# Optimization experiments

Hardware: AMD Instinct MI355X
Metric: run time of the kernel (lower is better)

## Reference

```python
import jax, jax.numpy as jnp
import numpy as np

N_NODES = 100000
N_EDGES = 1600000
EMD_DIM = 64
EPS = 1e-12  # F.normalize eps


def setup_inputs() -> dict:
    key = jax.random.key(0)
    ks = jax.random.split(key, 7)
    x = jax.random.normal(ks[0], (N_NODES, EMD_DIM), dtype=jnp.float32)
    W = jax.random.normal(ks[1], (EMD_DIM, EMD_DIM), dtype=jnp.float32) * (1.0 / np.sqrt(EMD_DIM))
    b = jax.random.normal(ks[2], (EMD_DIM,), dtype=jnp.float32) * 0.02
    wc = jax.random.normal(ks[3], (EMD_DIM,), dtype=jnp.float32) * (1.0 / np.sqrt(EMD_DIM))
    bc = jax.random.normal(ks[4], (1,), dtype=jnp.float32) * 0.02
    src = jax.random.randint(ks[5], (N_EDGES,), 0, N_NODES, dtype=jnp.int32)
    dst = jax.random.randint(ks[6], (N_EDGES,), 0, N_NODES, dtype=jnp.int32)
    return {"x": x, "W": W, "b": b, "wc": wc, "bc": bc, "src": src, "dst": dst}


def reference(x, W, b, wc, bc, src, dst):
    # gnn2: DGL GraphConv(norm='none', activation=None):
    #   y = sum_{(u->v) in E} (x @ W)[u]  scattered into v, plus bias.
    y = x @ W                                   # [N, D] dense transform first (D small)
    msg = y[src]                                # [E, D] gather
    agg = jax.ops.segment_sum(msg, dst, num_segments=x.shape[0])  # [N, D] scatter-add
    h = agg + b
    # F.normalize(h, p=2, dim=1)
    norm = jnp.linalg.norm(h, axis=1, keepdims=True)
    h = h / jnp.maximum(norm, EPS)
    # dgl.mean_nodes -> mean over all nodes; classifier Linear(D, 1).squeeze(-1)
    graph_repr = jnp.mean(h, axis=0)            # [D]
    logits = graph_repr @ wc + bc[0]            # scalar
    # emb dict is just contiguous slices of h (h2dict); h carries all embeddings.
    return logits, h
```

## Files before the change

kernel.cpp:

```cpp
#include <hip/hip_runtime.h>

#define NN 100000
#define NE 1600000
#define D 64
#define NB ((NN + 255) / 256)
#define SCAN2_T 512

__global__ __launch_bounds__(256) void degree_hist(const int* __restrict__ dst,
                                                   int* __restrict__ deg) {
    const int n4 = NE / 4;
    for (int i = blockIdx.x * blockDim.x + threadIdx.x; i < n4;
         i += gridDim.x * blockDim.x) {
        const int4 d = reinterpret_cast<const int4*>(dst)[i];
        atomicAdd(&deg[d.x], 1);
        atomicAdd(&deg[d.y], 1);
        atomicAdd(&deg[d.z], 1);
        atomicAdd(&deg[d.w], 1);
    }
}

__global__ __launch_bounds__(256) void scan1(const int* __restrict__ deg,
                                             int* __restrict__ partial,
                                             int* __restrict__ blockSums) {
    const int t = threadIdx.x;
    const int i = blockIdx.x * 256 + t;
    const int lane = t & 63, wid = t >> 6;
    const int orig = (i < NN) ? deg[i] : 0;
    int v = orig;
#pragma unroll
    for (int off = 1; off < 64; off <<= 1) {
        int n = __shfl_up(v, off, 64);
        if (lane >= off) v += n;
    }
    __shared__ int wsum[4];
    if (lane == 63) wsum[wid] = v;
    __syncthreads();
    if (t == 0) {
        int s = 0;
#pragma unroll
        for (int w = 0; w < 4; ++w) { int tmp = wsum[w]; wsum[w] = s; s += tmp; }
    }
    __syncthreads();
    const int incl = v + wsum[wid];
    if (i < NN) partial[i] = incl - orig;
    if (t == 255) blockSums[blockIdx.x] = incl;
}

__global__ __launch_bounds__(SCAN2_T) void scan2(int* __restrict__ blockSums) {
    __shared__ int sm[SCAN2_T];
    const int t = threadIdx.x;
    const int orig = (t < NB) ? blockSums[t] : 0;
    sm[t] = orig;
    __syncthreads();
    for (int off = 1; off < SCAN2_T; off <<= 1) {
        int v = (t >= off) ? sm[t - off] : 0;
        __syncthreads();
        sm[t] += v;
        __syncthreads();
    }
    if (t < NB) blockSums[t] = sm[t] - orig;
}

__global__ __launch_bounds__(256) void scan3(const int* __restrict__ partial,
                                             const int* __restrict__ blockSums,
                                             int* __restrict__ offs,
                                             int* __restrict__ cursor) {
    const int i = blockIdx.x * 256 + threadIdx.x;
    if (i < NN) {
        const int o = partial[i] + blockSums[blockIdx.x];
        offs[i] = o;
        cursor[i] = o;
    }
}

__global__ __launch_bounds__(256) void bucket_fill(const int* __restrict__ src,
                                                   const int* __restrict__ dst,
                                                   int* __restrict__ cursor,
                                                   int* __restrict__ csr) {
    const int n4 = NE / 4;
    for (int i = blockIdx.x * blockDim.x + threadIdx.x; i < n4;
         i += gridDim.x * blockDim.x) {
        const int4 d = reinterpret_cast<const int4*>(dst)[i];
        const int4 s = reinterpret_cast<const int4*>(src)[i];
        __builtin_nontemporal_store(s.x, &csr[atomicAdd(&cursor[d.x], 1)]);
        __builtin_nontemporal_store(s.y, &csr[atomicAdd(&cursor[d.y], 1)]);
        __builtin_nontemporal_store(s.z, &csr[atomicAdd(&cursor[d.z], 1)]);
        __builtin_nontemporal_store(s.w, &csr[atomicAdd(&cursor[d.w], 1)]);
    }
}

__global__ __launch_bounds__(256) void gather_transform_norm(
        const float* __restrict__ x, const int* __restrict__ csr,
        const int* __restrict__ offs, const int* __restrict__ deg,
        const float* __restrict__ W, const float* __restrict__ b,
        float* __restrict__ h, float* __restrict__ colsum) {
    const int lane = threadIdx.x & 63;
    const int wid  = threadIdx.x >> 6;
    const int grp  = lane >> 4;
    const int sub  = lane & 15;

    __shared__ float Wt[64 * 65];
    __shared__ float smem[4][64];
    for (int idx = threadIdx.x; idx < 64 * 64; idx += 256) {
        const int k = idx >> 6, l = idx & 63;
        Wt[l * 65 + k] = W[idx];
    }
    __syncthreads();
    const float bj = b[lane];
    const float* wrow = &Wt[lane * 65];

    const int waveId = (blockIdx.x * blockDim.x + threadIdx.x) >> 6;
    const int nWaves = (gridDim.x * blockDim.x) >> 6;
    float csum = 0.f;
    for (int node = waveId; node < NN; node += nWaves) {
        const int start = offs[node];
        const int cnt   = deg[node];
        float ax = 0.f, ay = 0.f, az = 0.f, aw = 0.f;
        for (int c0 = 0; c0 < cnt; c0 += 64) {
            const int pos  = start + c0 + lane;
            const int idxv = (pos < NE) ? csr[pos] : 0;
            const int m = (cnt - c0 < 64) ? (cnt - c0) : 64;
#pragma unroll 4
            for (int j = 0; j < m; j += 4) {
                const int e = j + grp;
                const int s = __shfl(idxv, e, 64);
                if (e < m) {
                    const float4 v = *reinterpret_cast<const float4*>(
                        x + (size_t)s * D + 4 * sub);
                    ax += v.x; ay += v.y; az += v.z; aw += v.w;
                }
            }
        }
#pragma unroll
        for (int off = 16; off <= 32; off <<= 1) {
            ax += __shfl_xor(ax, off, 64);
            ay += __shfl_xor(ay, off, 64);
            az += __shfl_xor(az, off, 64);
            aw += __shfl_xor(aw, off, 64);
        }
        float v = bj;
#pragma unroll
        for (int k0 = 0; k0 < 16; ++k0) {
            const float a0 = __shfl(ax, k0, 64);
            const float a1 = __shfl(ay, k0, 64);
            const float a2 = __shfl(az, k0, 64);
            const float a3 = __shfl(aw, k0, 64);
            v = fmaf(a0, wrow[4 * k0 + 0], v);
            v = fmaf(a1, wrow[4 * k0 + 1], v);
            v = fmaf(a2, wrow[4 * k0 + 2], v);
            v = fmaf(a3, wrow[4 * k0 + 3], v);
        }
        float ss = v * v;
#pragma unroll
        for (int off = 32; off > 0; off >>= 1) ss += __shfl_xor(ss, off, 64);
        v = v / fmaxf(sqrtf(ss), 1e-12f);
        __builtin_nontemporal_store(v, &h[(size_t)node * D + lane]);
        csum += v;
    }
    smem[wid][lane] = csum;
    __syncthreads();
    if (wid == 0) {
        const float t = smem[0][lane] + smem[1][lane] + smem[2][lane] + smem[3][lane];
        atomicAdd(&colsum[lane], t);
    }
}

__global__ void finalize(const float* __restrict__ colsum,
                         const float* __restrict__ wc,
                         const float* __restrict__ bc,
                         float* __restrict__ out0) {
    const int lane = threadIdx.x;
    float v = colsum[lane] * (1.0f / (float)NN) * wc[lane];
#pragma unroll
    for (int off = 32; off > 0; off >>= 1) v += __shfl_xor(v, off, 64);
    if (lane == 0) out0[0] = v + bc[0];
}

extern "C" void kernel_launch(void* const* d_in, const int* in_sizes, int n_in,
                              void* d_out, int out_size, void* d_ws, size_t ws_size,
                              hipStream_t stream) {
    const float* x   = (const float*)d_in[0];
    const float* W   = (const float*)d_in[1];
    const float* b   = (const float*)d_in[2];
    const float* wc  = (const float*)d_in[3];
    const float* bc  = (const float*)d_in[4];
    const int*   src = (const int*)d_in[5];
    const int*   dst = (const int*)d_in[6];

    float* out = (float*)d_out;
    float* h   = out + 1;

    int*   deg       = (int*)d_ws;
    int*   partial   = deg + NN;
    int*   offs      = partial + NN;
    int*   cursor    = offs + NN;
    int*   blockSums = cursor + NN;
    float* colsum    = (float*)(blockSums + SCAN2_T);
    int*   csr       = (int*)(colsum + 64);

    hipMemsetAsync(deg, 0, NN * sizeof(int), stream);
    hipMemsetAsync(colsum, 0, 64 * sizeof(float), stream);

    degree_hist<<<2048, 256, 0, stream>>>(dst, deg);
    scan1<<<NB, 256, 0, stream>>>(deg, partial, blockSums);
    scan2<<<1, SCAN2_T, 0, stream>>>(blockSums);
    scan3<<<NB, 256, 0, stream>>>(partial, blockSums, offs, cursor);
    bucket_fill<<<2048, 256, 0, stream>>>(src, dst, cursor, csr);
    gather_transform_norm<<<4096, 256, 0, stream>>>(x, csr, offs, deg, W, b, h, colsum);
    finalize<<<1, 64, 0, stream>>>(colsum, wc, bc, out);
}
```

Baseline: 438.3 us.

## Fuse CSR build phases into one cooperative kernel with grid syncs

Replaces the two memsets and five separate kernels (degree histogram, three-stage scan, bucket fill) with a single cooperative kernel of 512 blocks of 512 threads that separates the phases with grid.sync(). The aim is to remove per-launch overhead and inter-kernel gaps across the small phases. It also switches the nontemporal stores for csr and h to ordinary stores. In exchange, grid-wide barriers cost time, and the fixed grid gives less parallelism to the atomic-heavy phases than the earlier 2048-block launches.

```diff
diff --git a/kernel.cpp b/kernel.cpp
--- a/kernel.cpp
+++ b/kernel.cpp
@@ -1,91 +1,102 @@
 #include <hip/hip_runtime.h>
+#include <hip/hip_cooperative_groups.h>
+
+namespace cg = cooperative_groups;
 
 #define NN 100000
 #define NE 1600000
 #define D 64
-#define NB ((NN + 255) / 256)
-#define SCAN2_T 512
-
-__global__ __launch_bounds__(256) void degree_hist(const int* __restrict__ dst,
-                                                   int* __restrict__ deg) {
-    const int n4 = NE / 4;
-    for (int i = blockIdx.x * blockDim.x + threadIdx.x; i < n4;
-         i += gridDim.x * blockDim.x) {
-        const int4 d = reinterpret_cast<const int4*>(dst)[i];
-        atomicAdd(&deg[d.x], 1);
-        atomicAdd(&deg[d.y], 1);
-        atomicAdd(&deg[d.z], 1);
-        atomicAdd(&deg[d.w], 1);
-    }
-}
-
-__global__ __launch_bounds__(256) void scan1(const int* __restrict__ deg,
-                                             int* __restrict__ partial,
-                                             int* __restrict__ blockSums) {
+#define CB 512
+#define CG 512
+#define NCH ((NN + CB - 1) / CB)
+
+__global__ __launch_bounds__(CB) void build_csr(
+        const int* __restrict__ src, const int* __restrict__ dst,
+        int* __restrict__ deg, int* __restrict__ partial,
+        int* __restrict__ bsum, int* __restrict__ offs,
+        int* __restrict__ cursor, int* __restrict__ csr,
+        float* __restrict__ colsum) {
+    cg::grid_group grid = cg::this_grid();
     const int t = threadIdx.x;
-    const int i = blockIdx.x * 256 + t;
-    const int lane = t & 63, wid = t >> 6;
-    const int orig = (i < NN) ? deg[i] : 0;
-    int v = orig;
-#pragma unroll
-    for (int off = 1; off < 64; off <<= 1) {
-        int n = __shfl_up(v, off, 64);
-        if (lane >= off) v += n;
-    }
-    __shared__ int wsum[4];
-    if (lane == 63) wsum[wid] = v;
-    __syncthreads();
-    if (t == 0) {
-        int s = 0;
-#pragma unroll
-        for (int w = 0; w < 4; ++w) { int tmp = wsum[w]; wsum[w] = s; s += tmp; }
-    }
-    __syncthreads();
-    const int incl = v + wsum[wid];
-    if (i < NN) partial[i] = incl - orig;
-    if (t == 255) blockSums[blockIdx.x] = incl;
-}
-
-__global__ __launch_bounds__(SCAN2_T) void scan2(int* __restrict__ blockSums) {
-    __shared__ int sm[SCAN2_T];
-    const int t = threadIdx.x;
-    const int orig = (t < NB) ? blockSums[t] : 0;
-    sm[t] = orig;
-    __syncthreads();
-    for (int off = 1; off < SCAN2_T; off <<= 1) {
-        int v = (t >= off) ? sm[t - off] : 0;
+    const int gtid = blockIdx.x * CB + t;
+    const int gsz = CG * CB;
+
+    for (int i = gtid; i < NN; i += gsz) deg[i] = 0;
+    if (gtid < 64) colsum[gtid] = 0.f;
+    grid.sync();
+
+    {
+        const int n4 = NE / 4;
+        for (int i = gtid; i < n4; i += gsz) {
+            const int4 d4 = reinterpret_cast<const int4*>(dst)[i];
+            atomicAdd(&deg[d4.x], 1);
+            atomicAdd(&deg[d4.y], 1);
+            atomicAdd(&deg[d4.z], 1);
+            atomicAdd(&deg[d4.w], 1);
+        }
+    }
+    grid.sync();
+
+    if (blockIdx.x < NCH) {
+        const int i = blockIdx.x * CB + t;
+        const int lane = t & 63, wid = t >> 6;
+        const int orig = (i < NN) ? deg[i] : 0;
+        int v = orig;
+#pragma unroll
+        for (int off = 1; off < 64; off <<= 1) {
+            int n = __shfl_up(v, off, 64);
+            if (lane >= off) v += n;
+        }
+        __shared__ int wsum[8];
+        if (lane == 63) wsum[wid] = v;
         __syncthreads();
-        sm[t] += v;
+        if (t == 0) {
+            int s = 0;
+#pragma unroll
+            for (int w = 0; w < 8; ++w) { int tmp = wsum[w]; wsum[w] = s; s += tmp; }
+        }
         __syncthreads();
-    }
-    if (t < NB) blockSums[t] = sm[t] - orig;
-}
-
-__global__ __launch_bounds__(256) void scan3(const int* __restrict__ partial,
-                                             const int* __restrict__ blockSums,
-                                             int* __restrict__ offs,
-                                             int* __restrict__ cursor) {
-    const int i = blockIdx.x * 256 + threadIdx.x;
-    if (i < NN) {
-        const int o = partial[i] + blockSums[blockIdx.x];
-        offs[i] = o;
-        cursor[i] = o;
-    }
-}
-
-__global__ __launch_bounds__(256) void bucket_fill(const int* __restrict__ src,
-                                                   const int* __restrict__ dst,
-                                                   int* __restrict__ cursor,
-                                                   int* __restrict__ csr) {
-    const int n4 = NE / 4;
-    for (int i = blockIdx.x * blockDim.x + threadIdx.x; i < n4;
-         i += gridDim.x * blockDim.x) {
-        const int4 d = reinterpret_cast<const int4*>(dst)[i];
-        const int4 s = reinterpret_cast<const int4*>(src)[i];
-        __builtin_nontemporal_store(s.x, &csr[atomicAdd(&cursor[d.x], 1)]);
-        __builtin_nontemporal_store(s.y, &csr[atomicAdd(&cursor[d.y], 1)]);
-        __builtin_nontemporal_store(s.z, &csr[atomicAdd(&cursor[d.z], 1)]);
-        __builtin_nontemporal_store(s.w, &csr[atomicAdd(&cursor[d.w], 1)]);
+        const int incl = v + wsum[wid];
+        if (i < NN) partial[i] = incl - orig;
+        if (t == CB - 1) bsum[blockIdx.x] = incl;
+    }
+    grid.sync();
+
+    if (blockIdx.x == 0) {
+        __shared__ int sm[CB];
+        const int orig = (t < NCH) ? bsum[t] : 0;
+        sm[t] = orig;
+        __syncthreads();
+        for (int off = 1; off < CB; off <<= 1) {
+            const int v = (t >= off) ? sm[t - off] : 0;
+            __syncthreads();
+            sm[t] += v;
+            __syncthreads();
+        }
+        if (t < NCH) bsum[t] = sm[t] - orig;
+    }
+    grid.sync();
+
+    if (blockIdx.x < NCH) {
+        const int i = blockIdx.x * CB + t;
+        if (i < NN) {
+            const int o = partial[i] + bsum[blockIdx.x];
+            offs[i] = o;
+            cursor[i] = o;
+        }
+    }
+    grid.sync();
+
+    {
+        const int n4 = NE / 4;
+        for (int i = gtid; i < n4; i += gsz) {
+            const int4 d4 = reinterpret_cast<const int4*>(dst)[i];
+            const int4 s4 = reinterpret_cast<const int4*>(src)[i];
+            csr[atomicAdd(&cursor[d4.x], 1)] = s4.x;
+            csr[atomicAdd(&cursor[d4.y], 1)] = s4.y;
+            csr[atomicAdd(&cursor[d4.z], 1)] = s4.z;
+            csr[atomicAdd(&cursor[d4.w], 1)] = s4.w;
+        }
     }
 }
 
@@ -154,7 +165,7 @@
 #pragma unroll
         for (int off = 32; off > 0; off >>= 1) ss += __shfl_xor(ss, off, 64);
         v = v / fmaxf(sqrtf(ss), 1e-12f);
-        __builtin_nontemporal_store(v, &h[(size_t)node * D + lane]);
+        h[(size_t)node * D + lane] = v;
         csum += v;
     }
     smem[wid][lane] = csum;
@@ -190,22 +201,20 @@
     float* out = (float*)d_out;
     float* h   = out + 1;
 
-    int*   deg       = (int*)d_ws;
-    int*   partial   = deg + NN;
-    int*   offs      = partial + NN;
-    int*   cursor    = offs + NN;
-    int*   blockSums = cursor + NN;
-    float* colsum    = (float*)(blockSums + SCAN2_T);
-    int*   csr       = (int*)(colsum + 64);
-
-    hipMemsetAsync(deg, 0, NN * sizeof(int), stream);
-    hipMemsetAsync(colsum, 0, 64 * sizeof(float), stream);
-
-    degree_hist<<<2048, 256, 0, stream>>>(dst, deg);
-    scan1<<<NB, 256, 0, stream>>>(deg, partial, blockSums);
-    scan2<<<1, SCAN2_T, 0, stream>>>(blockSums);
-    scan3<<<NB, 256, 0, stream>>>(partial, blockSums, offs, cursor);
-    bucket_fill<<<2048, 256, 0, stream>>>(src, dst, cursor, csr);
+    int*   deg    = (int*)d_ws;
+    int*   partial= deg + NN;
+    int*   offs   = partial + NN;
+    int*   cursor = offs + NN;
+    int*   bsum   = cursor + NN;
+    float* colsum = (float*)(bsum + CB);
+    int*   csr    = (int*)(colsum + 64);
+
+    void* args[] = {(void*)&src, (void*)&dst, (void*)&deg, (void*)&partial,
+                    (void*)&bsum, (void*)&offs, (void*)&cursor, (void*)&csr,
+                    (void*)&colsum};
+    hipLaunchCooperativeKernel(reinterpret_cast<void*>(build_csr),
+                               dim3(CG), dim3(CB), args, 0, stream);
+
     gather_transform_norm<<<4096, 256, 0, stream>>>(x, csr, offs, deg, W, b, h, colsum);
     finalize<<<1, 64, 0, stream>>>(colsum, wc, bc, out);
 }
```

After: 685.1 us. 56.3% more time.
